# Performance work log

Hardware: AMD Instinct MI355X
Metric: run time of the kernel (lower is better)

## Reference

```python
import jax, jax.numpy as jnp
import numpy as np

N_NODES = 50000
N_EDGES = 800000
IN_CH = 128
HID = 128
OUT_CH = 16
N_LAYERS = 3
N_GRAPHS = 128
BN_EPS = 1e-5


def setup_inputs() -> dict:
    key = jax.random.key(0)
    ks = jax.random.split(key, 12)
    x = jax.random.normal(ks[0], (N_NODES, IN_CH), dtype=jnp.float32)
    edge_index = jax.random.randint(ks[1], (2, N_EDGES), 0, N_NODES, dtype=jnp.int64)
    batch = jnp.sort(jax.random.randint(ks[2], (N_NODES,), 0, N_GRAPHS, dtype=jnp.int64))
    s = 1.0 / np.sqrt(HID)
    W1 = jax.random.normal(ks[3], (N_LAYERS, IN_CH, HID), dtype=jnp.float32) * s
    b1 = jax.random.normal(ks[4], (N_LAYERS, HID), dtype=jnp.float32) * s
    W2 = jax.random.normal(ks[5], (N_LAYERS, HID, HID), dtype=jnp.float32) * s
    b2 = jax.random.normal(ks[6], (N_LAYERS, HID), dtype=jnp.float32) * s
    gamma = jnp.ones((N_LAYERS, HID), dtype=jnp.float32)
    beta = jnp.zeros((N_LAYERS, HID), dtype=jnp.float32)
    mean = jax.random.normal(ks[7], (N_LAYERS, HID), dtype=jnp.float32) * 0.1
    var = jax.random.uniform(ks[8], (N_LAYERS, HID), dtype=jnp.float32, minval=0.5, maxval=1.5)
    Wc = jax.random.normal(ks[9], (HID, OUT_CH), dtype=jnp.float32) * s
    bc = jax.random.normal(ks[10], (OUT_CH,), dtype=jnp.float32) * s
    return {"x": x, "edge_index": edge_index, "batch": batch, "W1": W1, "b1": b1,
            "W2": W2, "b2": b2, "gamma": gamma, "beta": beta, "mean": mean,
            "var": var, "Wc": Wc, "bc": bc}


def reference(x, edge_index, batch, W1, b1, W2, b2, gamma, beta, mean, var, Wc, bc):
    # GIN (eval mode: BN uses running stats, dropout is identity).
    src, dst = edge_index[0], edge_index[1]
    n = x.shape[0]
    h = x
    for i in range(N_LAYERS):
        # GINConv with eps=0: MLP(x + sum_{j->i} x_j)
        agg = jax.ops.segment_sum(h[src], dst, num_segments=n)  # [N, d]
        z = h + agg
        z = jnp.maximum(z @ W1[i] + b1[i], 0.0) @ W2[i] + b2[i]  # 2-layer MLP
        # BatchNorm1d (eval) + ReLU
        inv = gamma[i] * jax.lax.rsqrt(var[i] + BN_EPS)
        h = jnp.maximum((z - mean[i]) * inv + beta[i], 0.0)
    pooled = jax.ops.segment_sum(h, batch, num_segments=N_GRAPHS)  # [G, hid]
    return pooled @ Wc + bc
```

## Files before the change

### kernel.cpp

```cpp
#include <hip/hip_runtime.h>

#define N_NODES 50000
#define N_EDGES 800000
#define CH 128
#define N_GRAPHS 128
#define N_LAYERS 3
#define OUT_CH 16
#define BN_EPS 1e-5f
#define ZN N_NODES
#define NB 196
#define BCAP 4608
#define EPB 4096
#define NTILES (N_NODES / 16)
#define SSTRIDE 20
#define CB 6250
#define PB 388

typedef unsigned short ushort_t;
typedef __attribute__((ext_vector_type(8))) short bf16x8;
typedef __attribute__((ext_vector_type(4))) float f32x4;

__device__ inline ushort_t f2b(float f) {
    unsigned u = __float_as_uint(f);
    unsigned r = (u + 0x7fffu + ((u >> 16) & 1u)) >> 16;
    return (ushort_t)r;
}
__device__ inline float blo(unsigned u) { return __uint_as_float(u << 16); }
__device__ inline float bhi(unsigned u) { return __uint_as_float(u & 0xffff0000u); }

__global__ __launch_bounds__(256) void setup_kernel(
    const float4* __restrict__ x, ushort4* __restrict__ xb, ushort4* __restrict__ xz,
    int* __restrict__ gcur, float* __restrict__ pooled,
    const float* __restrict__ W1, const float* __restrict__ W2, ushort_t* __restrict__ Wt,
    const float* __restrict__ b1, const float* __restrict__ b2,
    const float* __restrict__ gamma, const float* __restrict__ beta,
    const float* __restrict__ mean, const float* __restrict__ var,
    float* __restrict__ scale, float* __restrict__ shift) {
    int bid = blockIdx.x, t = threadIdx.x;
    if (bid < CB) {
        int i = bid * 256 + t;
        if (i < NB) gcur[i] = 0;
        if (i < N_GRAPHS * CH) pooled[i] = 0.f;
        if (bid == 0 && t < 32) {
            ushort4 zz; zz.x = 0; zz.y = 0; zz.z = 0; zz.w = 0;
            xb[(size_t)ZN * 32 + t] = zz;
            xz[(size_t)ZN * 32 + t] = zz;
        }
        float4 v = x[i];
        ushort4 o;
        o.x = f2b(v.x); o.y = f2b(v.y); o.z = f2b(v.z); o.w = f2b(v.w);
        xb[i] = o;
    } else {
        int i = (bid - CB) * 256 + t;
        if (i < 6 * CH * CH) {
            int mat = i >> 14, r = i & 16383;
            int j = r & 7, bb = r >> 3;
            int lane = bb & 63, cs = bb >> 6;
            int ct = cs >> 2, ks = cs & 3;
            int n = ct * 16 + (lane & 15);
            int k = ks * 32 + (lane >> 4) * 8 + j;
            const float* Wsrc = (mat < 3) ? (W1 + (size_t)mat * CH * CH)
                                          : (W2 + (size_t)(mat - 3) * CH * CH);
            Wt[i] = f2b(Wsrc[k * CH + n]);
        } else {
            int e = i - 6 * CH * CH;
            if (e >= 6 * CH) return;
            int mat = e / CH, c = e % CH;
            if (mat < 3) {
                scale[e] = 1.f;
                shift[e] = b1[mat * CH + c];
            } else {
                int l = mat - 3;
                float inv = gamma[l * CH + c] * rsqrtf(var[l * CH + c] + BN_EPS);
                scale[e] = inv;
                shift[e] = (b2[l * CH + c] - mean[l * CH + c]) * inv + beta[l * CH + c];
            }
        }
    }
}

__global__ __launch_bounds__(256) void bin_kernel(const int* __restrict__ src,
                                                  const int* __restrict__ dst,
                                                  int* __restrict__ gcur,
                                                  unsigned* __restrict__ gbuck) {
    __shared__ int lcnt[256];
    __shared__ int lpref[256];
    __shared__ int lpos[NB];
    __shared__ int lbase[NB];
    __shared__ unsigned stage[EPB];
    __shared__ unsigned char sbk[EPB];
    int t = threadIdx.x;
    int e0 = blockIdx.x * EPB;
    int nloc = N_EDGES - e0; if (nloc > EPB) nloc = EPB;

    lcnt[t] = 0;
    __syncthreads();

    int2 ed[16];
    #pragma unroll
    for (int j = 0; j < 16; ++j) {
        int i = j * 256 + t;
        if (i < nloc) {
            ed[j].x = src[e0 + i];
            ed[j].y = dst[e0 + i];
            atomicAdd(&lcnt[ed[j].y >> 8], 1);
        } else ed[j].y = -1;
    }
    __syncthreads();
    int v = lcnt[t];
    lpref[t] = v;
    __syncthreads();
    for (int off = 1; off < 256; off <<= 1) {
        int y = (t >= off) ? lpref[t - off] : 0;
        __syncthreads();
        lpref[t] += y;
        __syncthreads();
    }
    int excl = lpref[t] - v;
    __syncthreads();
    lpref[t] = excl;
    if (t < NB) {
        lpos[t] = excl;
        lbase[t] = atomicAdd(&gcur[t], v);
    }
    __syncthreads();
    #pragma unroll
    for (int j = 0; j < 16; ++j) {
        if (ed[j].y >= 0) {
            int b = ed[j].y >> 8;
            int slot = atomicAdd(&lpos[b], 1);
            stage[slot] = (unsigned)ed[j].x | ((unsigned)(ed[j].y & 255) << 16);
            sbk[slot] = (unsigned char)b;
        }
    }
    __syncthreads();
    for (int i = t; i < nloc; i += 256) {
        int b = sbk[i];
        gbuck[(size_t)b * BCAP + lbase[b] + (i - lpref[b])] = stage[i];
    }
}

__global__ __launch_bounds__(256) void place_kernel(const int* __restrict__ gcur,
                                                    const unsigned* __restrict__ gbuck,
                                                    int* __restrict__ rowptr,
                                                    ushort_t* __restrict__ esrc) {
    __shared__ ushort_t ssrc[BCAP];
    __shared__ unsigned char sd[BCAP];
    __shared__ int outS[BCAP];
    __shared__ int cnt[256], pref[256], cur[256];
    __shared__ int sscan[256];
    int b = blockIdx.x, t = threadIdx.x;
    int gv = (t < NB) ? gcur[t] : 0;
    sscan[t] = gv;
    cnt[t] = 0;
    __syncthreads();
    for (int off = 1; off < 256; off <<= 1) {
        int y = (t >= off) ? sscan[t - off] : 0;
        __syncthreads();
        sscan[t] += y;
        __syncthreads();
    }
    int nb = gcur[b];
    int base = sscan[b] - nb;
    for (int i = t; i < nb; i += 256) {
        unsigned p = gbuck[(size_t)b * BCAP + i];
        ssrc[i] = (ushort_t)(p & 0xffffu);
        int dl = (p >> 16) & 0xff;
        sd[i] = (unsigned char)dl;
        atomicAdd(&cnt[dl], 1);
    }
    __syncthreads();
    int v = cnt[t];
    pref[t] = v;
    __syncthreads();
    for (int off = 1; off < 256; off <<= 1) {
        int y = (t >= off) ? pref[t - off] : 0;
        __syncthreads();
        pref[t] += y;
        __syncthreads();
    }
    int excl = pref[t] - v;
    __syncthreads();
    pref[t] = excl;
    cur[t] = 0;
    int idx = (b << 8) + t;
    if (idx < N_NODES) rowptr[idx] = base + excl;
    if (b == NB - 1 && t == 0) rowptr[N_NODES] = N_EDGES;
    __syncthreads();
    for (int i = t; i < nb; i += 256) {
        int dl = sd[i];
        int p = pref[dl] + atomicAdd(&cur[dl], 1);
        outS[p] = ssrc[i];
    }
    __syncthreads();
    for (int i = t; i < nb; i += 256)
        esrc[base + i] = (ushort_t)outS[i];
}

__global__ __launch_bounds__(512, 8) void layer_kernel(
    const unsigned* __restrict__ h2, const int* __restrict__ rowptr,
    const ushort_t* __restrict__ esrc,
    const ushort_t* __restrict__ Wf1, const ushort_t* __restrict__ Wf2,
    const float* __restrict__ shift1, const float* __restrict__ scale2,
    const float* __restrict__ shift2, ushort_t* __restrict__ hout,
    const int* __restrict__ batch, float* __restrict__ pooled, int do_pool) {
    __shared__ unsigned zt[16][68];
    __shared__ ushort_t sS[CH * SSTRIDE];

    int t = threadIdx.x;
    int wave = t >> 6, lane = t & 63;
    int quad = lane >> 4, l16 = lane & 15;
    int row0 = blockIdx.x * 16;

    for (int nn = 0; nn < 2; ++nn) {
        int node = row0 + wave * 2 + nn;
        unsigned self = h2[(size_t)node * 64 + lane];
        float ax = blo(self), ay = bhi(self);
        int e = rowptr[node], end = rowptr[node + 1];
        while (e < end) {
            unsigned u[16];
            #pragma unroll
            for (int j = 0; j < 16; ++j) {
                int raw = esrc[e + j];
                int s = (e + j < end) ? raw : ZN;
                u[j] = h2[(size_t)s * 64 + lane];
            }
            #pragma unroll
            for (int j = 0; j < 16; ++j) { ax += blo(u[j]); ay += bhi(u[j]); }
            e += 16;
        }
        zt[wave * 2 + nn][lane] = ((unsigned)f2b(ay) << 16) | (unsigned)f2b(ax);
    }
    __syncthreads();

    {
        bf16x8 af[4];
        #pragma unroll
        for (int ks = 0; ks < 4; ++ks)
            af[ks] = *(const bf16x8*)((const ushort_t*)&zt[l16][0] + ks * 32 + quad * 8);
        bf16x8 w1[4];
        #pragma unroll
        for (int ks = 0; ks < 4; ++ks)
            w1[ks] = *(const bf16x8*)(Wf1 + ((size_t)(wave * 4 + ks) * 64 + lane) * 8);
        f32x4 acc = (f32x4){0.f, 0.f, 0.f, 0.f};
        #pragma unroll
        for (int ks = 0; ks < 4; ++ks)
            acc = __builtin_amdgcn_mfma_f32_16x16x32_bf16(af[ks], w1[ks], acc, 0, 0, 0);
        int k = wave * 16 + l16;
        float sh = shift1[k];
        uint2 p;
        p.x = ((unsigned)f2b(fmaxf(acc[1] + sh, 0.f)) << 16)
            |  (unsigned)f2b(fmaxf(acc[0] + sh, 0.f));
        p.y = ((unsigned)f2b(fmaxf(acc[3] + sh, 0.f)) << 16)
            |  (unsigned)f2b(fmaxf(acc[2] + sh, 0.f));
        *(uint2*)&sS[k * SSTRIDE + quad * 4] = p;
    }
    __syncthreads();

    {
        bf16x8 af2[4];
        #pragma unroll
        for (int ks = 0; ks < 4; ++ks)
            #pragma unroll
            for (int j = 0; j < 8; ++j)
                af2[ks][j] = (short)sS[(ks * 32 + quad * 8 + j) * SSTRIDE + l16];
        bf16x8 w2[4];
        #pragma unroll
        for (int ks = 0; ks < 4; ++ks)
            w2[ks] = *(const bf16x8*)(Wf2 + ((size_t)(wave * 4 + ks) * 64 + lane) * 8);
        f32x4 acc = (f32x4){0.f, 0.f, 0.f, 0.f};
        #pragma unroll
        for (int ks = 0; ks < 4; ++ks)
            acc = __builtin_amdgcn_mfma_f32_16x16x32_bf16(af2[ks], w2[ks], acc, 0, 0, 0);
        int col = wave * 16 + l16;
        float sc = scale2[col], sh = shift2[col];
        float hv[4];
        #pragma unroll
        for (int r = 0; r < 4; ++r)
            hv[r] = fmaxf(acc[r] * sc + sh, 0.f);
        if (!do_pool) {
            #pragma unroll
            for (int r = 0; r < 4; ++r) {
                int row = row0 + quad * 4 + r;
                hout[(size_t)row * CH + col] = f2b(hv[r]);
            }
        } else {
            int g0 = batch[row0], g15 = batch[row0 + 15];
            if (g0 == g15) {
                float s = hv[0] + hv[1] + hv[2] + hv[3];
                s += __shfl_xor(s, 16);
                s += __shfl_xor(s, 32);
                if (quad == 0) atomicAdd(&pooled[g0 * CH + col], s);
            } else {
                #pragma unroll
                for (int r = 0; r < 4; ++r) {
                    int row = row0 + quad * 4 + r;
                    atomicAdd(&pooled[batch[row] * CH + col], hv[r]);
                }
            }
        }
    }
}

__global__ __launch_bounds__(256) void cls_kernel(const float* __restrict__ pooled,
                                                  const float* __restrict__ Wc,
                                                  const float* __restrict__ bc,
                                                  float* __restrict__ out) {
    int i = blockIdx.x * blockDim.x + threadIdx.x;
    if (i >= N_GRAPHS * OUT_CH) return;
    int g = i / OUT_CH, o = i % OUT_CH;
    float s = bc[o];
    for (int k = 0; k < CH; ++k) s += pooled[g * CH + k] * Wc[k * OUT_CH + o];
    out[i] = s;
}

extern "C" void kernel_launch(void* const* d_in, const int* in_sizes, int n_in,
                              void* d_out, int out_size, void* d_ws, size_t ws_size,
                              hipStream_t stream) {
    const float* x     = (const float*)d_in[0];
    const int*   eidx  = (const int*)d_in[1];
    const int*   batch = (const int*)d_in[2];
    const float* W1    = (const float*)d_in[3];
    const float* b1    = (const float*)d_in[4];
    const float* W2    = (const float*)d_in[5];
    const float* b2    = (const float*)d_in[6];
    const float* gamma = (const float*)d_in[7];
    const float* beta  = (const float*)d_in[8];
    const float* mean  = (const float*)d_in[9];
    const float* var   = (const float*)d_in[10];
    const float* Wc    = (const float*)d_in[11];
    const float* bc    = (const float*)d_in[12];
    float* out = (float*)d_out;

    const int* src = eidx;
    const int* dst = eidx + N_EDGES;

    char* w = (char*)d_ws;
    size_t off = 0;
    auto alloc = [&](size_t bytes) { void* p = w + off; off += (bytes + 255) & ~(size_t)255; return p; };
    int*      gcur   = (int*)alloc(NB * 4);
    unsigned* gbuck  = (unsigned*)alloc((size_t)NB * BCAP * 4);
    int*      rowptr = (int*)alloc((N_NODES + 1) * 4);
    ushort_t* esrc   = (ushort_t*)alloc(N_EDGES * 2);
    ushort_t* Bh     = (ushort_t*)alloc((size_t)(N_NODES + 1) * CH * 2);
    ushort_t* Bz     = (ushort_t*)alloc((size_t)(N_NODES + 1) * CH * 2);
    ushort_t* Wt     = (ushort_t*)alloc((size_t)6 * CH * CH * 2);
    float*    scale  = (float*)alloc(6 * CH * 4);
    float*    shift  = (float*)alloc(6 * CH * 4);
    float*    pooled = (float*)alloc(N_GRAPHS * CH * 4);
    (void)ws_size; (void)n_in; (void)in_sizes; (void)out_size;

    setup_kernel<<<CB + PB, 256, 0, stream>>>(
        (const float4*)x, (ushort4*)Bh, (ushort4*)Bz, gcur, pooled,
        W1, W2, Wt, b1, b2, gamma, beta, mean, var, scale, shift);
    bin_kernel<<<(N_EDGES + EPB - 1) / EPB, 256, 0, stream>>>(src, dst, gcur, gbuck);
    place_kernel<<<NB, 256, 0, stream>>>(gcur, gbuck, rowptr, esrc);

    ushort_t* bufA = Bh;
    ushort_t* bufB = Bz;
    for (int i = 0; i < N_LAYERS; ++i) {
        int last = (i == N_LAYERS - 1);
        layer_kernel<<<NTILES, 512, 0, stream>>>((const unsigned*)bufA, rowptr, esrc,
                                                 Wt + (size_t)i * CH * CH,
                                                 Wt + (size_t)(3 + i) * CH * CH,
                                                 shift + i * CH,
                                                 scale + (3 + i) * CH,
                                                 shift + (3 + i) * CH,
                                                 bufB, batch, pooled, last);
        ushort_t* tmp = bufA; bufA = bufB; bufB = tmp;
    }

    cls_kernel<<<(N_GRAPHS * OUT_CH + 255) / 256, 256, 0, stream>>>(pooled, Wc, bc, out);
}
```

Before: 242.0 us.

## Pad per-node edge lists to multiples of 16 and vector-load indices

Each node's edge list is now padded to a multiple of 16 with dummy zero-row indices and placed at a fixed per-bucket region. The row pointer packs the offset and the round count into one word, and the global prefix scan across buckets is dropped. The aggregation loop loads 16 source indices with two 16-byte vector loads and needs no bounds check. In exchange it gathers extra padded zero rows and uses more index memory.

```diff
diff --git a/kernel.cpp b/kernel.cpp
--- a/kernel.cpp
+++ b/kernel.cpp
@@ -10,6 +10,7 @@
 #define ZN N_NODES
 #define NB 196
 #define BCAP 4608
+#define PBCAP 8448
 #define EPB 4096
 #define NTILES (N_NODES / 16)
 #define SSTRIDE 20
@@ -18,6 +19,7 @@
 
 typedef unsigned short ushort_t;
 typedef __attribute__((ext_vector_type(8))) short bf16x8;
+typedef __attribute__((ext_vector_type(8))) unsigned short u16x8;
 typedef __attribute__((ext_vector_type(4))) float f32x4;
 
 __device__ inline ushort_t f2b(float f) {
@@ -146,22 +148,12 @@
                                                     ushort_t* __restrict__ esrc) {
     __shared__ ushort_t ssrc[BCAP];
     __shared__ unsigned char sd[BCAP];
-    __shared__ int outS[BCAP];
+    __shared__ ushort_t outS[PBCAP];
     __shared__ int cnt[256], pref[256], cur[256];
-    __shared__ int sscan[256];
     int b = blockIdx.x, t = threadIdx.x;
-    int gv = (t < NB) ? gcur[t] : 0;
-    sscan[t] = gv;
     cnt[t] = 0;
     __syncthreads();
-    for (int off = 1; off < 256; off <<= 1) {
-        int y = (t >= off) ? sscan[t - off] : 0;
-        __syncthreads();
-        sscan[t] += y;
-        __syncthreads();
-    }
     int nb = gcur[b];
-    int base = sscan[b] - nb;
     for (int i = t; i < nb; i += 256) {
         unsigned p = gbuck[(size_t)b * BCAP + i];
         ssrc[i] = (ushort_t)(p & 0xffffu);
@@ -171,7 +163,8 @@
     }
     __syncthreads();
     int v = cnt[t];
-    pref[t] = v;
+    int pc = (v + 15) & ~15;
+    pref[t] = pc;
     __syncthreads();
     for (int off = 1; off < 256; off <<= 1) {
         int y = (t >= off) ? pref[t - off] : 0;
@@ -179,13 +172,16 @@
         pref[t] += y;
         __syncthreads();
     }
-    int excl = pref[t] - v;
+    int excl = pref[t] - pc;
+    int total = pref[255];
     __syncthreads();
     pref[t] = excl;
     cur[t] = 0;
     int idx = (b << 8) + t;
-    if (idx < N_NODES) rowptr[idx] = base + excl;
-    if (b == NB - 1 && t == 0) rowptr[N_NODES] = N_EDGES;
+    if (idx < N_NODES)
+        rowptr[idx] = (b * PBCAP + excl) | ((pc >> 4) << 24);
+    __syncthreads();
+    for (int i = t; i < total; i += 256) outS[i] = (ushort_t)ZN;
     __syncthreads();
     for (int i = t; i < nb; i += 256) {
         int dl = sd[i];
@@ -193,8 +189,8 @@
         outS[p] = ssrc[i];
     }
     __syncthreads();
-    for (int i = t; i < nb; i += 256)
-        esrc[base + i] = (ushort_t)outS[i];
+    for (int i = t; i < total; i += 256)
+        esrc[(size_t)b * PBCAP + i] = outS[i];
 }
 
 __global__ __launch_bounds__(512, 8) void layer_kernel(
@@ -216,18 +212,21 @@
         int node = row0 + wave * 2 + nn;
         unsigned self = h2[(size_t)node * 64 + lane];
         float ax = blo(self), ay = bhi(self);
-        int e = rowptr[node], end = rowptr[node + 1];
-        while (e < end) {
+        int pr = rowptr[node];
+        int e = pr & 0xFFFFFF;
+        int rounds = (int)((unsigned)pr >> 24);
+        for (int r = 0; r < rounds; ++r, e += 16) {
+            u16x8 i0 = *(const u16x8*)(esrc + e);
+            u16x8 i1 = *(const u16x8*)(esrc + e + 8);
             unsigned u[16];
             #pragma unroll
-            for (int j = 0; j < 16; ++j) {
-                int raw = esrc[e + j];
-                int s = (e + j < end) ? raw : ZN;
-                u[j] = h2[(size_t)s * 64 + lane];
-            }
+            for (int j = 0; j < 8; ++j)
+                u[j] = h2[(size_t)i0[j] * 64 + lane];
+            #pragma unroll
+            for (int j = 0; j < 8; ++j)
+                u[8 + j] = h2[(size_t)i1[j] * 64 + lane];
             #pragma unroll
             for (int j = 0; j < 16; ++j) { ax += blo(u[j]); ay += bhi(u[j]); }
-            e += 16;
         }
         zt[wave * 2 + nn][lane] = ((unsigned)f2b(ay) << 16) | (unsigned)f2b(ax);
     }
@@ -340,8 +339,8 @@
     auto alloc = [&](size_t bytes) { void* p = w + off; off += (bytes + 255) & ~(size_t)255; return p; };
     int*      gcur   = (int*)alloc(NB * 4);
     unsigned* gbuck  = (unsigned*)alloc((size_t)NB * BCAP * 4);
-    int*      rowptr = (int*)alloc((N_NODES + 1) * 4);
-    ushort_t* esrc   = (ushort_t*)alloc(N_EDGES * 2);
+    int*      rowptr = (int*)alloc(N_NODES * 4);
+    ushort_t* esrc   = (ushort_t*)alloc((size_t)NB * PBCAP * 2);
     ushort_t* Bh     = (ushort_t*)alloc((size_t)(N_NODES + 1) * CH * 2);
     ushort_t* Bz     = (ushort_t*)alloc((size_t)(N_NODES + 1) * CH * 2);
     ushort_t* Wt     = (ushort_t*)alloc((size_t)6 * CH * CH * 2);
```

Result: faster. 230.4 us (-4.8%).
